# Kernel optimization log

Hardware: AMD Instinct MI355X
Metric: run time of the kernel (lower is better)

## Reference

```python
import jax, jax.numpy as jnp
import numpy as np
import math

B, S, D, H, HD = 2, 2048, 2048, 16, 128
ROPE_THETA = 10000.0


def _rope_cache(seq_len, dim, base, dtype=jnp.float32):
    inv_freq = 1.0 / (base ** (jnp.arange(0, dim, 2, dtype=jnp.float32) / dim))
    t = jnp.arange(seq_len, dtype=jnp.float32)
    freqs = jnp.einsum('i,j->ij', t, inv_freq)          # [S, dim/2]
    emb = jnp.concatenate([freqs, freqs], axis=-1)       # [S, dim]
    return jnp.cos(emb).astype(dtype), jnp.sin(emb).astype(dtype)


def _rotate_half(x):
    x1, x2 = x[..., : x.shape[-1] // 2], x[..., x.shape[-1] // 2:]
    return jnp.concatenate([-x2, x1], axis=-1)


def setup_inputs() -> dict:
    key = jax.random.key(0)
    ks = jax.random.split(key, 6)
    hidden_states = jax.random.normal(ks[0], (B, S, D), dtype=jnp.float32) * 0.02
    w_scale = 1.0 / math.sqrt(D)
    Wq = jax.random.normal(ks[1], (D, D), dtype=jnp.float32) * w_scale
    Wk = jax.random.normal(ks[2], (D, D), dtype=jnp.float32) * w_scale
    Wv = jax.random.normal(ks[3], (D, D), dtype=jnp.float32) * w_scale
    Wo = jax.random.normal(ks[4], (D, D), dtype=jnp.float32) * w_scale
    # additive causal mask [B, 1, S, S]: 0 on/below diag, large negative above
    causal = jnp.tril(jnp.ones((S, S), dtype=bool))
    attention_mask = jnp.where(causal, 0.0, -1e9).astype(jnp.float32)
    attention_mask = jnp.broadcast_to(attention_mask[None, None], (B, 1, S, S))
    position_ids = jnp.broadcast_to(jnp.arange(S, dtype=jnp.int32)[None], (B, S))
    return {
        'hidden_states': hidden_states,
        'attention_mask': attention_mask,
        'position_ids': position_ids,
        'Wq': Wq, 'Wk': Wk, 'Wv': Wv, 'Wo': Wo,
    }


def reference(hidden_states, attention_mask, position_ids, Wq, Wk, Wv, Wo):
    bsz, q_len, _ = hidden_states.shape
    # projections (torch Linear: x @ W.T), then split heads -> [B, H, S, HD]
    def proj(W):
        return jnp.einsum('bsd,ed->bse', hidden_states, W).reshape(bsz, q_len, H, HD).transpose(0, 2, 1, 3)
    q, k, v = proj(Wq), proj(Wk), proj(Wv)
    cos_c, sin_c = _rope_cache(q_len, HD, ROPE_THETA, hidden_states.dtype)
    cos = cos_c[position_ids][:, None]  # [B, 1, S, HD]
    sin = sin_c[position_ids][:, None]
    q = q * cos + _rotate_half(q) * sin
    k = k * cos + _rotate_half(k) * sin
    scores = jnp.einsum('bhqd,bhkd->bhqk', q, k) / math.sqrt(HD)
    scores = scores + attention_mask
    attn_weights = jax.nn.softmax(scores.astype(jnp.float32), axis=-1).astype(q.dtype)
    attn_out = jnp.einsum('bhqk,bhkd->bhqd', attn_weights, v)
    attn_out = attn_out.transpose(0, 2, 1, 3).reshape(bsz, q_len, D)
    out = jnp.einsum('bsd,ed->bse', attn_out, Wo)
    return out
```

## Files before the change

### kernel.cpp

```cpp
#include <hip/hip_runtime.h>

typedef __bf16 bf16;
typedef __bf16 bf16x8 __attribute__((ext_vector_type(8)));
typedef float f32x4 __attribute__((ext_vector_type(4)));

#define D_MODEL 2048
#define SEQ 2048
#define NH 16
#define HEAD_DIM 128
#define NBATCH 2
#define SM_SCALE 0.08838834764831845f
#define WSEG 4194304
#define NT_TILES 32

typedef __attribute__((address_space(1))) const void* gas_cp;
typedef __attribute__((address_space(3))) void* las_p;
__device__ __forceinline__ void ll16(const bf16* g, bf16* l) {
  __builtin_amdgcn_global_load_lds((gas_cp)g, (las_p)l, 16, 0, 0);
}

__device__ __forceinline__ bf16x8 cvt8(const float* p) {
  float4 a = *(const float4*)p;
  float4 b = *(const float4*)(p + 4);
  bf16x8 v;
  v[0] = (bf16)a.x; v[1] = (bf16)a.y; v[2] = (bf16)a.z; v[3] = (bf16)a.w;
  v[4] = (bf16)b.x; v[5] = (bf16)b.y; v[6] = (bf16)b.z; v[7] = (bf16)b.w;
  return v;
}

__global__ __launch_bounds__(256)
void cvt_hidden(const float* __restrict__ src, bf16* __restrict__ dst) {
  size_t i = ((size_t)blockIdx.x * 256 + threadIdx.x) * 8;
  *(bf16x8*)(dst + i) = cvt8(src + i);
}

__global__ __launch_bounds__(256)
void cvt_weights(const float* __restrict__ w0, const float* __restrict__ w1,
                 const float* __restrict__ w2, const float* __restrict__ w3,
                 bf16* __restrict__ dst) {
  const float* src = (blockIdx.y == 0) ? w0 : (blockIdx.y == 1) ? w1
                   : (blockIdx.y == 2) ? w2 : w3;
  size_t i = ((size_t)blockIdx.x * 256 + threadIdx.x) * 8;
  *(bf16x8*)(dst + (size_t)blockIdx.y * WSEG + i) = cvt8(src + i);
}

#define LOADA(HB)                                                            \
  _Pragma("unroll") for (int mi = 0; mi < 2; mi++)                           \
  _Pragma("unroll") for (int ks = 0; ks < 2; ks++)                           \
      af[mi][ks] = *(const bf16x8*)((HB) + ((rowA + mi * 16) << 7) +         \
                                    (ks ? kx1 : kx0));

#define LOADB(HB)                                                            \
  _Pragma("unroll") for (int ks = 0; ks < 2; ks++) {                         \
    bfr[0][ks] = *(const bf16x8*)((HB) + (rb0 << 7) + (ks ? kx1 : kx0));     \
    bfr[1][ks] = *(const bf16x8*)((HB) + (rb1 << 7) + (ks ? kx1 : kx0));     \
    bfr[2][ks] = *(const bf16x8*)((HB) + (rb2 << 7) + (ks ? kx1 : kx0));     \
    bfr[3][ks] = *(const bf16x8*)((HB) + (rb3 << 7) + (ks ? kx1 : kx0));     \
  }

#define MMAC(QM, QN)                                                         \
  _Pragma("unroll") for (int ks = 0; ks < 2; ks++)                           \
  _Pragma("unroll") for (int mi = 0; mi < 2; mi++)                           \
  _Pragma("unroll") for (int ni = 0; ni < 4; ni++)                           \
      acc[QM][QN][mi][ni] = __builtin_amdgcn_mfma_f32_16x16x32_bf16(         \
          af[mi][ks], bfr[ni][ks], acc[QM][QN][mi][ni], 0, 0, 0);

#define STAGE(GP, ROW0, KT, LB)                                              \
  _Pragma("unroll") for (int i_ = 0; i_ < 2; i_++) {                         \
    ll16((GP) + (size_t)((ROW0) + (i_ * 8 + w) * 8 + l8) * D_MODEL +         \
             (KT) * 64 + kelem,                                              \
         (bf16*)((LB) + (i_ * 8 + w) * 1024));                               \
  }

#define PHASE_SYNC_PRE()                                                     \
  __builtin_amdgcn_s_barrier();                                              \
  asm volatile("s_waitcnt lgkmcnt(0)" ::: "memory");                         \
  __builtin_amdgcn_sched_barrier(0);                                         \
  __builtin_amdgcn_s_setprio(1);

#define PHASE_SYNC_POST()                                                    \
  __builtin_amdgcn_s_setprio(0);                                             \
  __builtin_amdgcn_s_barrier();

template <typename TC, int MODE, int NBN>
__global__ __launch_bounds__(512, 2)
void gemm8p(const bf16* __restrict__ A, const bf16* __restrict__ W,
            TC* __restrict__ C, bf16* __restrict__ Qo, bf16* __restrict__ Ko,
            bf16* __restrict__ Vo, const int* __restrict__ pos_ids) {
  __shared__ __align__(16) char smem[131072];

  const int tid  = threadIdx.x;
  const int lane = tid & 63;
  const int w    = tid >> 6;
  const int quad = lane >> 4, l15 = lane & 15;
  const int wr   = w >> 1;
  const int wc   = w & 1;
  const int l8   = lane >> 3, l7 = lane & 7;
  const int kelem = 8 * (l7 ^ l8);

  const int nwg = 16 * NBN;
  const int bid = blockIdx.x;
  const int lin = (bid & 7) * (nwg >> 3) + (bid >> 3);
  const int by = lin / NBN, bx = lin % NBN;
  const int mBase = by << 8, nBase = bx << 8;

  const int kx0 = (quad * 16) ^ ((l15 & 7) << 4);
  const int kx1 = kx0 ^ 64;
  const int rowA = wr * 32 + l15;
  const int rb0 = wc * 32 + l15, rb1 = rb0 + 16, rb2 = rb0 + 64, rb3 = rb0 + 80;

  f32x4 acc[2][2][2][4];
#pragma unroll
  for (int a = 0; a < 2; a++)
#pragma unroll
    for (int b = 0; b < 2; b++)
#pragma unroll
      for (int c = 0; c < 2; c++)
#pragma unroll
        for (int d = 0; d < 4; d++) acc[a][b][c][d] = 0.0f;

  bf16x8 af[2][2], bfr[4][2];

  {
    char* s = smem;
    STAGE(A, mBase,       0, s + 0);
    STAGE(A, mBase + 128, 0, s + 16384);
    STAGE(W, nBase,       0, s + 32768);
    STAGE(W, nBase + 128, 0, s + 49152);
    STAGE(W, nBase,       1, s + 65536 + 32768);
    STAGE(A, mBase + 128, 1, s + 65536 + 16384);
  }
  asm volatile("s_waitcnt vmcnt(4)" ::: "memory");
  __builtin_amdgcn_s_barrier();

  for (int t = 0; t < NT_TILES; ++t) {
    const int buf = t & 1;
    char* const A0  = smem + buf * 65536;
    char* const A1h = A0 + 16384;
    char* const B0  = A0 + 32768;
    char* const B1h = B0 + 16384;
    char* const oA0 = smem + (buf ^ 1) * 65536;
    char* const oB1 = oA0 + 32768 + 16384;

    LOADA(A0);
    LOADB(B0);
    if (t + 1 < NT_TILES) STAGE(A, mBase, t + 1, oA0);
    PHASE_SYNC_PRE();
    MMAC(0, 0);
    PHASE_SYNC_POST();

    LOADA(A1h);
    if (t + 1 < NT_TILES) STAGE(W, nBase + 128, t + 1, oB1);
    PHASE_SYNC_PRE();
    MMAC(1, 0);
    PHASE_SYNC_POST();

    LOADB(B1h);
    if (t + 2 < NT_TILES) STAGE(W, nBase, t + 2, B0);
    PHASE_SYNC_PRE();
    MMAC(1, 1);
    PHASE_SYNC_POST();

    LOADA(A0);
    if (t + 2 < NT_TILES) STAGE(A, mBase + 128, t + 2, A1h);
    __builtin_amdgcn_s_barrier();
    asm volatile("s_waitcnt lgkmcnt(0)" ::: "memory");
    __builtin_amdgcn_sched_barrier(0);
    __builtin_amdgcn_s_setprio(1);
    MMAC(0, 1);
    __builtin_amdgcn_s_setprio(0);
    if (t + 2 < NT_TILES)
      asm volatile("s_waitcnt vmcnt(4)" ::: "memory");
    else
      asm volatile("s_waitcnt vmcnt(0)" ::: "memory");
    __builtin_amdgcn_s_barrier();
  }

  if (MODE == 0) {
#pragma unroll
    for (int qm = 0; qm < 2; qm++)
#pragma unroll
      for (int qn = 0; qn < 2; qn++)
#pragma unroll
        for (int mi = 0; mi < 2; mi++)
#pragma unroll
          for (int ni = 0; ni < 4; ni++) {
            int n = nBase + qn * 128 + wc * 32 + (ni & 1) * 16 + (ni >> 1) * 64 + l15;
            int mb = mBase + qm * 128 + wr * 32 + mi * 16 + quad * 4;
            TC* cp = C + (size_t)mb * D_MODEL + n;
#pragma unroll
            for (int r = 0; r < 4; r++) cp[(size_t)r * D_MODEL] = (TC)acc[qm][qn][mi][ni][r];
          }
  } else {
    const int matrix = nBase >> 11;
    const int nb     = nBase & 2047;
    if (matrix == 2) {
#pragma unroll
      for (int qm = 0; qm < 2; qm++)
#pragma unroll
        for (int qn = 0; qn < 2; qn++) {
          const int h = (nb >> 7) + qn;
#pragma unroll
          for (int mi = 0; mi < 2; mi++)
#pragma unroll
            for (int ni = 0; ni < 4; ni++) {
              const int hd = wc * 32 + (ni & 1) * 16 + (ni >> 1) * 64 + l15;
#pragma unroll
              for (int r = 0; r < 4; r++) {
                int m = mBase + qm * 128 + wr * 32 + mi * 16 + quad * 4 + r;
                int b = m >> 11, s2 = m & 2047;
                Vo[((size_t)((b * NH + h) * HEAD_DIM + hd)) * SEQ + s2] =
                    (bf16)acc[qm][qn][mi][ni][r];
              }
            }
        }
    } else {
      bf16* Out = (matrix == 0) ? Qo : Ko;
      float invf[2];
#pragma unroll
      for (int ni = 0; ni < 2; ni++)
        invf[ni] = __expf(-(float)(wc * 32 + ni * 16 + l15) *
                          (9.210340371976184f / 64.0f));
#pragma unroll
      for (int qm = 0; qm < 2; qm++)
#pragma unroll
        for (int mi = 0; mi < 2; mi++)
#pragma unroll
          for (int r = 0; r < 4; r++) {
            int m = mBase + qm * 128 + wr * 32 + mi * 16 + quad * 4 + r;
            float pos = (float)pos_ids[m];
#pragma unroll
            for (int qn = 0; qn < 2; qn++) {
              bf16* op = Out + (size_t)m * D_MODEL + nb + qn * 128 + wc * 32 + l15;
#pragma unroll
              for (int ni = 0; ni < 2; ni++) {
                float sn, cs;
                __sincosf(pos * invf[ni], &sn, &cs);
                float q0 = acc[qm][qn][mi][ni][r];
                float q1 = acc[qm][qn][mi][ni + 2][r];
                op[ni * 16]      = (bf16)(q0 * cs - q1 * sn);
                op[ni * 16 + 64] = (bf16)(q1 * cs + q0 * sn);
              }
            }
          }
    }
  }
}

__global__ __launch_bounds__(256, 3)
void attn_mfma(const bf16* __restrict__ Q, const bf16* __restrict__ K,
               const bf16* __restrict__ Vt, bf16* __restrict__ O) {
  __shared__ __align__(16) bf16 K_lds[64 * 136];
  __shared__ __align__(16) bf16 V_lds[128 * 72];
  __shared__ __align__(16) bf16 P_lds[64 * 72];

  const int tid  = threadIdx.x;
  const int lane = tid & 63;
  const int w    = tid >> 6;
  const int quad = lane >> 4, l15 = lane & 15;
  const int s    = 31 - blockIdx.y;
  const int bh   = blockIdx.x;
  const size_t qkBase = (size_t)(bh >> 4) * SEQ * D_MODEL + (size_t)(bh & 15) * HEAD_DIM;
  const size_t vBase  = (size_t)bh * HEAD_DIM * SEQ;

  const int qbase = s * 64 + w * 16;

  bf16x8 qa[4];
#pragma unroll
  for (int kk = 0; kk < 4; kk++)
    qa[kk] = *(const bf16x8*)(Q + qkBase + (size_t)(qbase + l15) * D_MODEL + kk * 32 + quad * 8);

  bf16x8 ones;
#pragma unroll
  for (int i = 0; i < 8; i++) ones[i] = (bf16)1.0f;

  f32x4 oacc[8], ls;
#pragma unroll
  for (int ni = 0; ni < 8; ni++) oacc[ni] = 0.0f;
  ls = 0.0f;

  const int ntiles = s + 1;

  bf16x8 kr[4], vr[4];
  auto loadKV = [&](int t0) {
#pragma unroll
    for (int i = 0; i < 4; i++) {
      int c = tid + 256 * i;
      kr[i] = *(const bf16x8*)(K + qkBase + (size_t)(t0 + (c >> 4)) * D_MODEL + (c & 15) * 8);
    }
#pragma unroll
    for (int i = 0; i < 4; i++) {
      int c = tid + 256 * i;
      vr[i] = *(const bf16x8*)(Vt + vBase + (size_t)(c >> 3) * SEQ + t0 + (c & 7) * 8);
    }
  };
  loadKV(0);

  const int prow = w * 16;

  for (int tt = 0; tt < ntiles; tt++) {
    const int t0 = tt * 64;
    __syncthreads();
#pragma unroll
    for (int i = 0; i < 4; i++) {
      int c = tid + 256 * i;
      *(bf16x8*)&K_lds[(c >> 4) * 136 + (c & 15) * 8] = kr[i];
    }
#pragma unroll
    for (int i = 0; i < 4; i++) {
      int c = tid + 256 * i;
      *(bf16x8*)&V_lds[(c >> 3) * 72 + (c & 7) * 8] = vr[i];
    }
    __syncthreads();
    if (tt + 1 < ntiles) loadKV(t0 + 64);

    f32x4 sacc[4];
#pragma unroll
    for (int ni = 0; ni < 4; ni++) sacc[ni] = 0.0f;
#pragma unroll
    for (int kk = 0; kk < 4; kk++) {
#pragma unroll
      for (int ni = 0; ni < 4; ni++) {
        bf16x8 kf = *(const bf16x8*)&K_lds[(ni * 16 + l15) * 136 + kk * 32 + quad * 8];
        sacc[ni] = __builtin_amdgcn_mfma_f32_16x16x32_bf16(qa[kk], kf, sacc[ni], 0, 0, 0);
      }
    }

    if (tt == s) {
#pragma unroll
      for (int r = 0; r < 4; r++) {
        int qrow = qbase + quad * 4 + r;
#pragma unroll
        for (int ni = 0; ni < 4; ni++) {
          int tcol = t0 + ni * 16 + l15;
          float pv = (tcol <= qrow) ? __expf(fminf(sacc[ni][r] * SM_SCALE, 30.0f)) : 0.0f;
          P_lds[(prow + quad * 4 + r) * 72 + ni * 16 + l15] = (bf16)pv;
        }
      }
    } else {
#pragma unroll
      for (int r = 0; r < 4; r++)
#pragma unroll
        for (int ni = 0; ni < 4; ni++)
          P_lds[(prow + quad * 4 + r) * 72 + ni * 16 + l15] =
              (bf16)__expf(fminf(sacc[ni][r] * SM_SCALE, 30.0f));
    }

#pragma unroll
    for (int kk2 = 0; kk2 < 2; kk2++) {
      bf16x8 pf = *(const bf16x8*)&P_lds[(prow + l15) * 72 + kk2 * 32 + quad * 8];
#pragma unroll
      for (int ni = 0; ni < 8; ni++) {
        bf16x8 vf = *(const bf16x8*)&V_lds[(ni * 16 + l15) * 72 + kk2 * 32 + quad * 8];
        oacc[ni] = __builtin_amdgcn_mfma_f32_16x16x32_bf16(pf, vf, oacc[ni], 0, 0, 0);
      }
      ls = __builtin_amdgcn_mfma_f32_16x16x32_bf16(pf, ones, ls, 0, 0, 0);
    }
  }

#pragma unroll
  for (int r = 0; r < 4; r++) {
    float inv = 1.0f / ls[r];
    bf16* op = O + qkBase + (size_t)(qbase + quad * 4 + r) * D_MODEL;
#pragma unroll
    for (int ni = 0; ni < 8; ni++)
      op[ni * 16 + l15] = (bf16)(oacc[ni][r] * inv);
  }
}

extern "C" void kernel_launch(void* const* d_in, const int* in_sizes, int n_in,
                              void* d_out, int out_size, void* d_ws, size_t ws_size,
                              hipStream_t stream) {
  const float* hidden = (const float*)d_in[0];
  const int* pos = (const int*)d_in[2];
  const float* Wq = (const float*)d_in[3];
  const float* Wk = (const float*)d_in[4];
  const float* Wv = (const float*)d_in[5];
  const float* Wo = (const float*)d_in[6];
  float* out = (float*)d_out;

  const size_t TENS = (size_t)NBATCH * SEQ * D_MODEL;
  bf16* Qb = (bf16*)d_ws;
  bf16* Kb = Qb + TENS;
  bf16* Vt = Kb + TENS;
  bf16* AO = Vt + TENS;
  bf16* Hb = AO + TENS;
  bf16* Wb = Hb + TENS;

  cvt_hidden<<<dim3(TENS / 2048), dim3(256), 0, stream>>>(hidden, Hb);
  cvt_weights<<<dim3(WSEG / 2048, 4), dim3(256), 0, stream>>>(Wq, Wk, Wv, Wo, Wb);

  gemm8p<bf16, 1, 24><<<dim3(384), dim3(512), 0, stream>>>(
      Hb, Wb, (bf16*)nullptr, Qb, Kb, Vt, pos);

  attn_mfma<<<dim3(NBATCH * NH, 32), dim3(256), 0, stream>>>(Qb, Kb, Vt, AO);

  gemm8p<float, 0, 8><<<dim3(128), dim3(512), 0, stream>>>(
      AO, Wb + 3 * (size_t)WSEG, out, nullptr, nullptr, nullptr, nullptr);
}
```

Before: 389.0 us.

## Add 128x256-tile triple-buffered output projection GEMM and reuse A fragments

```diff
diff --git a/kernel.cpp b/kernel.cpp
--- a/kernel.cpp
+++ b/kernel.cpp
@@ -44,10 +44,10 @@
   *(bf16x8*)(dst + (size_t)blockIdx.y * WSEG + i) = cvt8(src + i);
 }
 
-#define LOADA(HB)                                                            \
+#define LOADA(HB, AF)                                                        \
   _Pragma("unroll") for (int mi = 0; mi < 2; mi++)                           \
   _Pragma("unroll") for (int ks = 0; ks < 2; ks++)                           \
-      af[mi][ks] = *(const bf16x8*)((HB) + ((rowA + mi * 16) << 7) +         \
+      AF[mi][ks] = *(const bf16x8*)((HB) + ((rowA + mi * 16) << 7) +         \
                                     (ks ? kx1 : kx0));
 
 #define LOADB(HB)                                                            \
@@ -58,12 +58,12 @@
     bfr[3][ks] = *(const bf16x8*)((HB) + (rb3 << 7) + (ks ? kx1 : kx0));     \
   }
 
-#define MMAC(QM, QN)                                                         \
+#define MMAC(QM, QN, AF)                                                     \
   _Pragma("unroll") for (int ks = 0; ks < 2; ks++)                           \
   _Pragma("unroll") for (int mi = 0; mi < 2; mi++)                           \
   _Pragma("unroll") for (int ni = 0; ni < 4; ni++)                           \
       acc[QM][QN][mi][ni] = __builtin_amdgcn_mfma_f32_16x16x32_bf16(         \
-          af[mi][ks], bfr[ni][ks], acc[QM][QN][mi][ni], 0, 0, 0);
+          AF[mi][ks], bfr[ni][ks], acc[QM][QN][mi][ni], 0, 0, 0);
 
 #define STAGE(GP, ROW0, KT, LB)                                              \
   _Pragma("unroll") for (int i_ = 0; i_ < 2; i_++) {                         \
@@ -119,7 +119,7 @@
 #pragma unroll
         for (int d = 0; d < 4; d++) acc[a][b][c][d] = 0.0f;
 
-  bf16x8 af[2][2], bfr[4][2];
+  bf16x8 afA[2][2], afB[2][2], bfr[4][2];
 
   {
     char* s = smem;
@@ -142,32 +142,31 @@
     char* const oA0 = smem + (buf ^ 1) * 65536;
     char* const oB1 = oA0 + 32768 + 16384;
 
-    LOADA(A0);
+    LOADA(A0, afA);
     LOADB(B0);
     if (t + 1 < NT_TILES) STAGE(A, mBase, t + 1, oA0);
     PHASE_SYNC_PRE();
-    MMAC(0, 0);
+    MMAC(0, 0, afA);
     PHASE_SYNC_POST();
 
-    LOADA(A1h);
+    LOADA(A1h, afB);
     if (t + 1 < NT_TILES) STAGE(W, nBase + 128, t + 1, oB1);
     PHASE_SYNC_PRE();
-    MMAC(1, 0);
+    MMAC(1, 0, afB);
     PHASE_SYNC_POST();
 
     LOADB(B1h);
     if (t + 2 < NT_TILES) STAGE(W, nBase, t + 2, B0);
     PHASE_SYNC_PRE();
-    MMAC(1, 1);
+    MMAC(1, 1, afB);
     PHASE_SYNC_POST();
 
-    LOADA(A0);
     if (t + 2 < NT_TILES) STAGE(A, mBase + 128, t + 2, A1h);
     __builtin_amdgcn_s_barrier();
     asm volatile("s_waitcnt lgkmcnt(0)" ::: "memory");
     __builtin_amdgcn_sched_barrier(0);
     __builtin_amdgcn_s_setprio(1);
-    MMAC(0, 1);
+    MMAC(0, 1, afA);
     __builtin_amdgcn_s_setprio(0);
     if (t + 2 < NT_TILES)
       asm volatile("s_waitcnt vmcnt(4)" ::: "memory");
@@ -247,6 +246,132 @@
   }
 }
 
+__global__ __launch_bounds__(512, 2)
+void gemm_proj(const bf16* __restrict__ A, const bf16* __restrict__ W,
+               float* __restrict__ C) {
+  __shared__ __align__(16) char smem[147456];
+
+  const int tid  = threadIdx.x;
+  const int lane = tid & 63;
+  const int w    = tid >> 6;
+  const int quad = lane >> 4, l15 = lane & 15;
+  const int l8   = lane >> 3, l7 = lane & 7;
+  const int kelem = 8 * (l7 ^ l8);
+  const int wr = w >> 2, wc = w & 3;
+
+  const int bid = blockIdx.x;
+  const int lin = (bid & 7) * 32 + (bid >> 3);
+  const int by = lin >> 3, bx = lin & 7;
+  const int mBase = by << 7, nBase = bx << 8;
+
+  const int kx0 = (quad * 16) ^ ((l15 & 7) << 4);
+  const int kx1 = kx0 ^ 64;
+  const int arow = wr * 64 + l15;
+  const int brow = wc * 64 + l15;
+
+  f32x4 acc[4][4];
+#pragma unroll
+  for (int i = 0; i < 4; i++)
+#pragma unroll
+    for (int j = 0; j < 4; j++) acc[i][j] = 0.0f;
+
+  bf16x8 af[4], bfr[4];
+
+#define ST1(GP, ROW0, KT, LB)                                                \
+  ll16((GP) + (size_t)((ROW0) + w * 8 + l8) * D_MODEL + (KT) * 64 + kelem,   \
+       (bf16*)((LB) + w * 1024));
+
+  {
+    char* s0 = smem;
+    char* s1 = smem + 49152;
+    ST1(A, mBase,       0, s0 + 0);
+    ST1(A, mBase + 64,  0, s0 + 8192);
+    ST1(W, nBase,       0, s0 + 16384);
+    ST1(W, nBase + 64,  0, s0 + 24576);
+    ST1(W, nBase + 128, 0, s0 + 32768);
+    ST1(W, nBase + 192, 0, s0 + 40960);
+    ST1(A, mBase,       1, s1 + 0);
+    ST1(A, mBase + 64,  1, s1 + 8192);
+    ST1(W, nBase,       1, s1 + 16384);
+    ST1(W, nBase + 64,  1, s1 + 24576);
+    ST1(W, nBase + 128, 1, s1 + 32768);
+    ST1(W, nBase + 192, 1, s1 + 40960);
+  }
+  asm volatile("s_waitcnt vmcnt(6)" ::: "memory");
+  __builtin_amdgcn_s_barrier();
+
+  int buf = 0;
+  for (int t = 0; t < NT_TILES; ++t) {
+    char* const Sb = smem + buf * 49152;
+    const int  pb  = (buf + 2 >= 3) ? buf - 1 : buf + 2;
+    char* const Pb = smem + pb * 49152;
+    const bool pf  = (t + 2 < NT_TILES);
+
+#pragma unroll
+    for (int mi = 0; mi < 4; mi++)
+      af[mi] = *(const bf16x8*)(Sb + ((arow + mi * 16) << 7) + kx0);
+#pragma unroll
+    for (int ni = 0; ni < 4; ni++)
+      bfr[ni] = *(const bf16x8*)(Sb + 16384 + ((brow + ni * 16) << 7) + kx0);
+    if (pf) {
+      ST1(A, mBase,      t + 2, Pb + 0);
+      ST1(A, mBase + 64, t + 2, Pb + 8192);
+      ST1(W, nBase,      t + 2, Pb + 16384);
+    }
+    PHASE_SYNC_PRE();
+#pragma unroll
+    for (int mi = 0; mi < 4; mi++)
+#pragma unroll
+      for (int ni = 0; ni < 4; ni++)
+        acc[mi][ni] = __builtin_amdgcn_mfma_f32_16x16x32_bf16(
+            af[mi], bfr[ni], acc[mi][ni], 0, 0, 0);
+    PHASE_SYNC_POST();
+
+#pragma unroll
+    for (int mi = 0; mi < 4; mi++)
+      af[mi] = *(const bf16x8*)(Sb + ((arow + mi * 16) << 7) + kx1);
+#pragma unroll
+    for (int ni = 0; ni < 4; ni++)
+      bfr[ni] = *(const bf16x8*)(Sb + 16384 + ((brow + ni * 16) << 7) + kx1);
+    if (pf) {
+      ST1(W, nBase + 64,  t + 2, Pb + 24576);
+      ST1(W, nBase + 128, t + 2, Pb + 32768);
+      ST1(W, nBase + 192, t + 2, Pb + 40960);
+    }
+    __builtin_amdgcn_s_barrier();
+    asm volatile("s_waitcnt lgkmcnt(0)" ::: "memory");
+    __builtin_amdgcn_sched_barrier(0);
+    __builtin_amdgcn_s_setprio(1);
+#pragma unroll
+    for (int mi = 0; mi < 4; mi++)
+#pragma unroll
+      for (int ni = 0; ni < 4; ni++)
+        acc[mi][ni] = __builtin_amdgcn_mfma_f32_16x16x32_bf16(
+            af[mi], bfr[ni], acc[mi][ni], 0, 0, 0);
+    __builtin_amdgcn_s_setprio(0);
+    if (pf)
+      asm volatile("s_waitcnt vmcnt(6)" ::: "memory");
+    else
+      asm volatile("s_waitcnt vmcnt(0)" ::: "memory");
+    __builtin_amdgcn_s_barrier();
+
+    buf = (buf == 2) ? 0 : buf + 1;
+  }
+#undef ST1
+
+#pragma unroll
+  for (int mi = 0; mi < 4; mi++) {
+    const int m = mBase + wr * 64 + mi * 16 + quad * 4;
+#pragma unroll
+    for (int ni = 0; ni < 4; ni++) {
+      const int n = nBase + wc * 64 + ni * 16 + l15;
+      float* cp = C + (size_t)m * D_MODEL + n;
+#pragma unroll
+      for (int r = 0; r < 4; r++) cp[(size_t)r * D_MODEL] = acc[mi][ni][r];
+    }
+  }
+}
+
 __global__ __launch_bounds__(256, 3)
 void attn_mfma(const bf16* __restrict__ Q, const bf16* __restrict__ K,
                const bf16* __restrict__ Vt, bf16* __restrict__ O) {
@@ -395,6 +520,6 @@
 
   attn_mfma<<<dim3(NBATCH * NH, 32), dim3(256), 0, stream>>>(Qb, Kb, Vt, AO);
 
-  gemm8p<float, 0, 8><<<dim3(128), dim3(512), 0, stream>>>(
-      AO, Wb + 3 * (size_t)WSEG, out, nullptr, nullptr, nullptr, nullptr);
-}
+  gemm_proj<<<dim3(256), dim3(512), 0, stream>>>(
+      AO, Wb + 3 * (size_t)WSEG, out);
+}
```

Result: faster. 376.8 us (-3.2%).

## Switch GEMMs to 128x256 tiles with a three-stage LDS pipeline

Applied to the files above, without the earlier changes.

```diff
diff --git a/kernel.cpp b/kernel.cpp
--- a/kernel.cpp
+++ b/kernel.cpp
@@ -44,34 +44,6 @@
   *(bf16x8*)(dst + (size_t)blockIdx.y * WSEG + i) = cvt8(src + i);
 }
 
-#define LOADA(HB)                                                            \
-  _Pragma("unroll") for (int mi = 0; mi < 2; mi++)                           \
-  _Pragma("unroll") for (int ks = 0; ks < 2; ks++)                           \
-      af[mi][ks] = *(const bf16x8*)((HB) + ((rowA + mi * 16) << 7) +         \
-                                    (ks ? kx1 : kx0));
-
-#define LOADB(HB)                                                            \
-  _Pragma("unroll") for (int ks = 0; ks < 2; ks++) {                         \
-    bfr[0][ks] = *(const bf16x8*)((HB) + (rb0 << 7) + (ks ? kx1 : kx0));     \
-    bfr[1][ks] = *(const bf16x8*)((HB) + (rb1 << 7) + (ks ? kx1 : kx0));     \
-    bfr[2][ks] = *(const bf16x8*)((HB) + (rb2 << 7) + (ks ? kx1 : kx0));     \
-    bfr[3][ks] = *(const bf16x8*)((HB) + (rb3 << 7) + (ks ? kx1 : kx0));     \
-  }
-
-#define MMAC(QM, QN)                                                         \
-  _Pragma("unroll") for (int ks = 0; ks < 2; ks++)                           \
-  _Pragma("unroll") for (int mi = 0; mi < 2; mi++)                           \
-  _Pragma("unroll") for (int ni = 0; ni < 4; ni++)                           \
-      acc[QM][QN][mi][ni] = __builtin_amdgcn_mfma_f32_16x16x32_bf16(         \
-          af[mi][ks], bfr[ni][ks], acc[QM][QN][mi][ni], 0, 0, 0);
-
-#define STAGE(GP, ROW0, KT, LB)                                              \
-  _Pragma("unroll") for (int i_ = 0; i_ < 2; i_++) {                         \
-    ll16((GP) + (size_t)((ROW0) + (i_ * 8 + w) * 8 + l8) * D_MODEL +         \
-             (KT) * 64 + kelem,                                              \
-         (bf16*)((LB) + (i_ * 8 + w) * 1024));                               \
-  }
-
 #define PHASE_SYNC_PRE()                                                     \
   __builtin_amdgcn_s_barrier();                                              \
   asm volatile("s_waitcnt lgkmcnt(0)" ::: "memory");                         \
@@ -84,165 +56,180 @@
 
 template <typename TC, int MODE, int NBN>
 __global__ __launch_bounds__(512, 2)
-void gemm8p(const bf16* __restrict__ A, const bf16* __restrict__ W,
-            TC* __restrict__ C, bf16* __restrict__ Qo, bf16* __restrict__ Ko,
-            bf16* __restrict__ Vo, const int* __restrict__ pos_ids) {
-  __shared__ __align__(16) char smem[131072];
+void gemm128(const bf16* __restrict__ A, const bf16* __restrict__ W,
+             TC* __restrict__ C, bf16* __restrict__ Qo, bf16* __restrict__ Ko,
+             bf16* __restrict__ Vo, const int* __restrict__ pos_ids) {
+  __shared__ __align__(16) char smem[147456];
 
   const int tid  = threadIdx.x;
   const int lane = tid & 63;
   const int w    = tid >> 6;
   const int quad = lane >> 4, l15 = lane & 15;
-  const int wr   = w >> 1;
-  const int wc   = w & 1;
   const int l8   = lane >> 3, l7 = lane & 7;
   const int kelem = 8 * (l7 ^ l8);
-
-  const int nwg = 16 * NBN;
+  const int wm = w >> 2;
+  const int wn = w & 3;
+  const int hh = wn >> 1;
+  const int cb = (wn & 1) * 32;
+
+  const int nwg = 32 * NBN;
   const int bid = blockIdx.x;
   const int lin = (bid & 7) * (nwg >> 3) + (bid >> 3);
   const int by = lin / NBN, bx = lin % NBN;
-  const int mBase = by << 8, nBase = bx << 8;
+  const int mBase = by << 7, nBase = bx << 8;
 
   const int kx0 = (quad * 16) ^ ((l15 & 7) << 4);
   const int kx1 = kx0 ^ 64;
-  const int rowA = wr * 32 + l15;
-  const int rb0 = wc * 32 + l15, rb1 = rb0 + 16, rb2 = rb0 + 64, rb3 = rb0 + 80;
-
-  f32x4 acc[2][2][2][4];
-#pragma unroll
-  for (int a = 0; a < 2; a++)
-#pragma unroll
-    for (int b = 0; b < 2; b++)
-#pragma unroll
-      for (int c = 0; c < 2; c++)
-#pragma unroll
-        for (int d = 0; d < 4; d++) acc[a][b][c][d] = 0.0f;
-
-  bf16x8 af[2][2], bfr[4][2];
+  const int arow = wm * 64 + l15;
+  const int rb0 = hh * 128 + cb + l15;
+  const int rb1 = rb0 + 16, rb2 = rb0 + 64, rb3 = rb0 + 80;
+
+  f32x4 acc[4][4];
+#pragma unroll
+  for (int i = 0; i < 4; i++)
+#pragma unroll
+    for (int j = 0; j < 4; j++) acc[i][j] = 0.0f;
+
+  bf16x8 af[4], bfr[4];
+
+#define ST1(GP, ROW0, KT, LB)                                                \
+  ll16((GP) + (size_t)((ROW0) + w * 8 + l8) * D_MODEL + (KT) * 64 + kelem,   \
+       (bf16*)((LB) + w * 1024));
 
   {
-    char* s = smem;
-    STAGE(A, mBase,       0, s + 0);
-    STAGE(A, mBase + 128, 0, s + 16384);
-    STAGE(W, nBase,       0, s + 32768);
-    STAGE(W, nBase + 128, 0, s + 49152);
-    STAGE(W, nBase,       1, s + 65536 + 32768);
-    STAGE(A, mBase + 128, 1, s + 65536 + 16384);
-  }
-  asm volatile("s_waitcnt vmcnt(4)" ::: "memory");
+    char* s0 = smem;
+    char* s1 = smem + 49152;
+    ST1(A, mBase,       0, s0 + 0);
+    ST1(A, mBase + 64,  0, s0 + 8192);
+    ST1(W, nBase,       0, s0 + 16384);
+    ST1(W, nBase + 64,  0, s0 + 24576);
+    ST1(W, nBase + 128, 0, s0 + 32768);
+    ST1(W, nBase + 192, 0, s0 + 40960);
+    ST1(A, mBase,       1, s1 + 0);
+    ST1(A, mBase + 64,  1, s1 + 8192);
+    ST1(W, nBase,       1, s1 + 16384);
+    ST1(W, nBase + 64,  1, s1 + 24576);
+    ST1(W, nBase + 128, 1, s1 + 32768);
+    ST1(W, nBase + 192, 1, s1 + 40960);
+  }
+  asm volatile("s_waitcnt vmcnt(6)" ::: "memory");
   __builtin_amdgcn_s_barrier();
 
+  int buf = 0;
   for (int t = 0; t < NT_TILES; ++t) {
-    const int buf = t & 1;
-    char* const A0  = smem + buf * 65536;
-    char* const A1h = A0 + 16384;
-    char* const B0  = A0 + 32768;
-    char* const B1h = B0 + 16384;
-    char* const oA0 = smem + (buf ^ 1) * 65536;
-    char* const oB1 = oA0 + 32768 + 16384;
-
-    LOADA(A0);
-    LOADB(B0);
-    if (t + 1 < NT_TILES) STAGE(A, mBase, t + 1, oA0);
+    char* const Sb = smem + buf * 49152;
+    const int  pb  = (buf + 2 >= 3) ? buf - 1 : buf + 2;
+    char* const Pb = smem + pb * 49152;
+    const bool pf  = (t + 2 < NT_TILES);
+
+#pragma unroll
+    for (int mi = 0; mi < 4; mi++)
+      af[mi] = *(const bf16x8*)(Sb + ((arow + mi * 16) << 7) + kx0);
+    bfr[0] = *(const bf16x8*)(Sb + 16384 + (rb0 << 7) + kx0);
+    bfr[1] = *(const bf16x8*)(Sb + 16384 + (rb1 << 7) + kx0);
+    bfr[2] = *(const bf16x8*)(Sb + 16384 + (rb2 << 7) + kx0);
+    bfr[3] = *(const bf16x8*)(Sb + 16384 + (rb3 << 7) + kx0);
+    if (pf) {
+      ST1(A, mBase,      t + 2, Pb + 0);
+      ST1(A, mBase + 64, t + 2, Pb + 8192);
+      ST1(W, nBase,      t + 2, Pb + 16384);
+    }
     PHASE_SYNC_PRE();
-    MMAC(0, 0);
+#pragma unroll
+    for (int mi = 0; mi < 4; mi++)
+#pragma unroll
+      for (int ni = 0; ni < 4; ni++)
+        acc[mi][ni] = __builtin_amdgcn_mfma_f32_16x16x32_bf16(
+            af[mi], bfr[ni], acc[mi][ni], 0, 0, 0);
     PHASE_SYNC_POST();
 
-    LOADA(A1h);
-    if (t + 1 < NT_TILES) STAGE(W, nBase + 128, t + 1, oB1);
-    PHASE_SYNC_PRE();
-    MMAC(1, 0);
-    PHASE_SYNC_POST();
-
-    LOADB(B1h);
-    if (t + 2 < NT_TILES) STAGE(W, nBase, t + 2, B0);
-    PHASE_SYNC_PRE();
-    MMAC(1, 1);
-    PHASE_SYNC_POST();
-
-    LOADA(A0);
-    if (t + 2 < NT_TILES) STAGE(A, mBase + 128, t + 2, A1h);
+#pragma unroll
+    for (int mi = 0; mi < 4; mi++)
+      af[mi] = *(const bf16x8*)(Sb + ((arow + mi * 16) << 7) + kx1);
+    bfr[0] = *(const bf16x8*)(Sb + 16384 + (rb0 << 7) + kx1);
+    bfr[1] = *(const bf16x8*)(Sb + 16384 + (rb1 << 7) + kx1);
+    bfr[2] = *(const bf16x8*)(Sb + 16384 + (rb2 << 7) + kx1);
+    bfr[3] = *(const bf16x8*)(Sb + 16384 + (rb3 << 7) + kx1);
+    if (pf) {
+      ST1(W, nBase + 64,  t + 2, Pb + 24576);
+      ST1(W, nBase + 128, t + 2, Pb + 32768);
+      ST1(W, nBase + 192, t + 2, Pb + 40960);
+    }
     __builtin_amdgcn_s_barrier();
     asm volatile("s_waitcnt lgkmcnt(0)" ::: "memory");
     __builtin_amdgcn_sched_barrier(0);
     __builtin_amdgcn_s_setprio(1);
-    MMAC(0, 1);
+#pragma unroll
+    for (int mi = 0; mi < 4; mi++)
+#pragma unroll
+      for (int ni = 0; ni < 4; ni++)
+        acc[mi][ni] = __builtin_amdgcn_mfma_f32_16x16x32_bf16(
+            af[mi], bfr[ni], acc[mi][ni], 0, 0, 0);
     __builtin_amdgcn_s_setprio(0);
-    if (t + 2 < NT_TILES)
-      asm volatile("s_waitcnt vmcnt(4)" ::: "memory");
+    if (pf)
+      asm volatile("s_waitcnt vmcnt(6)" ::: "memory");
     else
       asm volatile("s_waitcnt vmcnt(0)" ::: "memory");
     __builtin_amdgcn_s_barrier();
-  }
+
+    buf = (buf == 2) ? 0 : buf + 1;
+  }
+#undef ST1
 
   if (MODE == 0) {
 #pragma unroll
-    for (int qm = 0; qm < 2; qm++)
-#pragma unroll
-      for (int qn = 0; qn < 2; qn++)
-#pragma unroll
-        for (int mi = 0; mi < 2; mi++)
-#pragma unroll
-          for (int ni = 0; ni < 4; ni++) {
-            int n = nBase + qn * 128 + wc * 32 + (ni & 1) * 16 + (ni >> 1) * 64 + l15;
-            int mb = mBase + qm * 128 + wr * 32 + mi * 16 + quad * 4;
-            TC* cp = C + (size_t)mb * D_MODEL + n;
-#pragma unroll
-            for (int r = 0; r < 4; r++) cp[(size_t)r * D_MODEL] = (TC)acc[qm][qn][mi][ni][r];
-          }
+    for (int mi = 0; mi < 4; mi++) {
+      const int m = mBase + wm * 64 + mi * 16 + quad * 4;
+#pragma unroll
+      for (int ni = 0; ni < 4; ni++) {
+        const int n = nBase + hh * 128 + cb + (ni & 1) * 16 + (ni >> 1) * 64 + l15;
+        TC* cp = C + (size_t)m * D_MODEL + n;
+#pragma unroll
+        for (int r = 0; r < 4; r++) cp[(size_t)r * D_MODEL] = (TC)acc[mi][ni][r];
+      }
+    }
   } else {
     const int matrix = nBase >> 11;
     const int nb     = nBase & 2047;
     if (matrix == 2) {
-#pragma unroll
-      for (int qm = 0; qm < 2; qm++)
-#pragma unroll
-        for (int qn = 0; qn < 2; qn++) {
-          const int h = (nb >> 7) + qn;
-#pragma unroll
-          for (int mi = 0; mi < 2; mi++)
-#pragma unroll
-            for (int ni = 0; ni < 4; ni++) {
-              const int hd = wc * 32 + (ni & 1) * 16 + (ni >> 1) * 64 + l15;
-#pragma unroll
-              for (int r = 0; r < 4; r++) {
-                int m = mBase + qm * 128 + wr * 32 + mi * 16 + quad * 4 + r;
-                int b = m >> 11, s2 = m & 2047;
-                Vo[((size_t)((b * NH + h) * HEAD_DIM + hd)) * SEQ + s2] =
-                    (bf16)acc[qm][qn][mi][ni][r];
-              }
-            }
+      const int h = (nb >> 7) + hh;
+#pragma unroll
+      for (int mi = 0; mi < 4; mi++)
+#pragma unroll
+        for (int ni = 0; ni < 4; ni++) {
+          const int hd = cb + (ni & 1) * 16 + (ni >> 1) * 64 + l15;
+#pragma unroll
+          for (int r = 0; r < 4; r++) {
+            int m = mBase + wm * 64 + mi * 16 + quad * 4 + r;
+            int b = m >> 11, s2 = m & 2047;
+            Vo[((size_t)((b * NH + h) * HEAD_DIM + hd)) * SEQ + s2] =
+                (bf16)acc[mi][ni][r];
+          }
         }
     } else {
       bf16* Out = (matrix == 0) ? Qo : Ko;
       float invf[2];
 #pragma unroll
       for (int ni = 0; ni < 2; ni++)
-        invf[ni] = __expf(-(float)(wc * 32 + ni * 16 + l15) *
+        invf[ni] = __expf(-(float)(cb + ni * 16 + l15) *
                           (9.210340371976184f / 64.0f));
 #pragma unroll
-      for (int qm = 0; qm < 2; qm++)
-#pragma unroll
-        for (int mi = 0; mi < 2; mi++)
-#pragma unroll
-          for (int r = 0; r < 4; r++) {
-            int m = mBase + qm * 128 + wr * 32 + mi * 16 + quad * 4 + r;
-            float pos = (float)pos_ids[m];
-#pragma unroll
-            for (int qn = 0; qn < 2; qn++) {
-              bf16* op = Out + (size_t)m * D_MODEL + nb + qn * 128 + wc * 32 + l15;
-#pragma unroll
-              for (int ni = 0; ni < 2; ni++) {
-                float sn, cs;
-                __sincosf(pos * invf[ni], &sn, &cs);
-                float q0 = acc[qm][qn][mi][ni][r];
-                float q1 = acc[qm][qn][mi][ni + 2][r];
-                op[ni * 16]      = (bf16)(q0 * cs - q1 * sn);
-                op[ni * 16 + 64] = (bf16)(q1 * cs + q0 * sn);
-              }
-            }
+      for (int mi = 0; mi < 4; mi++)
+#pragma unroll
+        for (int r = 0; r < 4; r++) {
+          int m = mBase + wm * 64 + mi * 16 + quad * 4 + r;
+          float pos = (float)pos_ids[m];
+          bf16* op = Out + (size_t)m * D_MODEL + nb + hh * 128 + cb + l15;
+#pragma unroll
+          for (int ni = 0; ni < 2; ni++) {
+            float sn, cs;
+            __sincosf(pos * invf[ni], &sn, &cs);
+            float q0 = acc[mi][ni][r];
+            float q1 = acc[mi][ni + 2][r];
+            op[ni * 16]      = (bf16)(q0 * cs - q1 * sn);
+            op[ni * 16 + 64] = (bf16)(q1 * cs + q0 * sn);
           }
+        }
     }
   }
 }
@@ -390,11 +377,11 @@
   cvt_hidden<<<dim3(TENS / 2048), dim3(256), 0, stream>>>(hidden, Hb);
   cvt_weights<<<dim3(WSEG / 2048, 4), dim3(256), 0, stream>>>(Wq, Wk, Wv, Wo, Wb);
 
-  gemm8p<bf16, 1, 24><<<dim3(384), dim3(512), 0, stream>>>(
+  gemm128<bf16, 1, 24><<<dim3(768), dim3(512), 0, stream>>>(
       Hb, Wb, (bf16*)nullptr, Qb, Kb, Vt, pos);
 
   attn_mfma<<<dim3(NBATCH * NH, 32), dim3(256), 0, stream>>>(Qb, Kb, Vt, AO);
 
-  gemm8p<float, 0, 8><<<dim3(128), dim3(512), 0, stream>>>(
+  gemm128<float, 0, 8><<<dim3(256), dim3(512), 0, stream>>>(
       AO, Wb + 3 * (size_t)WSEG, out, nullptr, nullptr, nullptr, nullptr);
 }
```

After: 382.0 us. Within noise of the previous version (-1.8%).
